# Kernel optimization log

Measured on AMD Instinct MI355X. Metric: run time of the kernel, lower is better.

Reference implementation:

```python
import jax, jax.numpy as jnp
import numpy as np

N, E, IN, H1, H2, C = 50000, 800000, 256, 64, 64, 40
NEG_SLOPE = 0.2


def _glorot(key, shape):
    fan_in = shape[0]
    return jax.random.normal(key, shape, jnp.float32) / np.sqrt(fan_in)


def gat_conv(x, W, al, ar, src, dst, act):
    """DGL-style GATConv (no bias, no residual). al/ar: [H, D]."""
    n = x.shape[0]
    H, D = al.shape
    feat = (x @ W).reshape(n, H, D)                      # [N,H,D]
    el = jnp.sum(feat * al, axis=-1)                     # [N,H]
    er = jnp.sum(feat * ar, axis=-1)                     # [N,H]
    e = jax.nn.leaky_relu(el[src] + er[dst], NEG_SLOPE)  # [E,H]
    # edge softmax over incoming edges of each dst node
    emax = jax.ops.segment_max(e, dst, num_segments=n)
    emax = jnp.where(jnp.isfinite(emax), emax, 0.0)      # guard zero-in-degree
    ex = jnp.exp(e - emax[dst])
    den = jax.ops.segment_sum(ex, dst, num_segments=n)
    alpha = ex / jnp.maximum(den[dst], 1e-9)             # [E,H]
    msg = feat[src] * alpha[..., None]                   # [E,H,D]
    rst = jax.ops.segment_sum(msg, dst, num_segments=n)  # [N,H,D]
    return act(rst) if act is not None else rst


def setup_inputs() -> dict:
    key = jax.random.key(0)
    ks = jax.random.split(key, 24)
    x = jax.random.normal(ks[0], (N, IN), jnp.float32)
    src = jax.random.randint(ks[1], (E,), 0, N, jnp.int32)
    dst = jax.random.randint(ks[2], (E,), 0, N, jnp.int32)
    p = {
        # branch 0 (even): GAT(num_layers=2, heads=[4,1,1])
        "W00": _glorot(ks[3], (IN, 4 * H1)),  "a00l": _glorot(ks[4], (4, H1)),  "a00r": _glorot(ks[5], (4, H1)),
        "W01": _glorot(ks[6], (4 * H1, H1)),  "a01l": _glorot(ks[7], (1, H1)),  "a01r": _glorot(ks[8], (1, H1)),
        "W0f": _glorot(ks[9], (H1, C)),       "a0fl": _glorot(ks[10], (1, C)),  "a0fr": _glorot(ks[11], (1, C)),
        # branch 1 (odd): GAT(num_layers=1, heads=[4,1]) encoder + 1-head output conv
        "W10": _glorot(ks[12], (IN, 4 * H2)), "a10l": _glorot(ks[13], (4, H2)), "a10r": _glorot(ks[14], (4, H2)),
        "W1f": _glorot(ks[15], (4 * H2, H1)), "a1fl": _glorot(ks[16], (1, H1)), "a1fr": _glorot(ks[17], (1, H1)),
        "W1o": _glorot(ks[18], (H1, C)),      "a1ol": _glorot(ks[19], (1, C)),  "a1or": _glorot(ks[20], (1, C)),
    }
    return {"x": x, "src": src, "dst": dst, **p}


def reference(x, src, dst,
              W00, a00l, a00r, W01, a01l, a01r, W0f, a0fl, a0fr,
              W10, a10l, a10r, W1f, a1fl, a1fr, W1o, a1ol, a1or):
    elu = jax.nn.elu
    n = x.shape[0]
    # branch 0: stacked GAT, final layer mean over heads, no activation
    h = gat_conv(x, W00, a00l, a00r, src, dst, elu).reshape(n, -1)   # [N,4*H1]
    h = gat_conv(h, W01, a01l, a01r, src, dst, elu).reshape(n, -1)   # [N,H1]
    y0 = gat_conv(h, W0f, a0fl, a0fr, src, dst, None).mean(axis=1)   # [N,C]
    # branch 1: encoder GAT -> emb, then 1-head output conv with elu
    h = gat_conv(x, W10, a10l, a10r, src, dst, elu).reshape(n, -1)   # [N,4*H2]
    emb = gat_conv(h, W1f, a1fl, a1fr, src, dst, None).mean(axis=1)  # [N,H1]
    y1 = gat_conv(emb, W1o, a1ol, a1or, src, dst, elu)[:, 0, :]      # [N,C]
    return jnp.stack([y0, y1], axis=0)                               # [2,N,C]
```

## Files before the change

### kernel.cpp

```cpp
#include <hip/hip_runtime.h>
#include <math.h>

typedef __attribute__((ext_vector_type(8))) short bf16x8;
typedef __attribute__((ext_vector_type(4))) float f32x4;

#define FMAMIX_LO(acc, pk, s) \
    asm("v_fma_mix_f32 %0, %1, %2, %0 op_sel:[0,0,0] op_sel_hi:[1,0,0]" \
        : "+v"(acc) : "v"(pk), "v"(s))
#define FMAMIX_HI(acc, pk, s) \
    asm("v_fma_mix_f32 %0, %1, %2, %0 op_sel:[1,0,0] op_sel_hi:[1,0,0]" \
        : "+v"(acc) : "v"(pk), "v"(s))

__device__ __forceinline__ unsigned short f2bf(float f) {
    unsigned int u = __float_as_uint(f);
    unsigned int r = (u + 0x7FFF + ((u >> 16) & 1)) >> 16;
    return (unsigned short)r;
}
__device__ __forceinline__ float bf2f(unsigned short h) {
    return __uint_as_float((unsigned int)h << 16);
}
__device__ __forceinline__ void split_bf(float x, unsigned short& hi, unsigned short& lo) {
    hi = f2bf(x);
    lo = f2bf(x - bf2f(hi));
}


__global__ void k_hist(const int* __restrict__ dst, int* __restrict__ deg, int e) {
    int t = blockIdx.x * 256 + threadIdx.x;
    if (t < e) atomicAdd(&deg[dst[t]], 1);
}

__global__ void k_scan1(const int* __restrict__ deg, int* __restrict__ tmp,
                        int* __restrict__ bsum, int n) {
    __shared__ int s[1024];
    int t = threadIdx.x;
    int g = blockIdx.x * 1024 + t;
    int v = (g < n) ? deg[g] : 0;
    s[t] = v;
    __syncthreads();
    for (int off = 1; off < 1024; off <<= 1) {
        int u = (t >= off) ? s[t - off] : 0;
        __syncthreads();
        s[t] += u;
        __syncthreads();
    }
    if (g < n) tmp[g] = s[t];
    if (t == 1023) bsum[blockIdx.x] = s[t];
}

__global__ void k_scan2(int* bsum, int nb) {
    int acc = 0;
    for (int b = 0; b < nb; ++b) { int v = bsum[b]; bsum[b] = acc; acc += v; }
}

__global__ void k_scan3(const int* __restrict__ deg, const int* __restrict__ tmp,
                        const int* __restrict__ bsum, int* __restrict__ rowptr,
                        int* __restrict__ cursor, int n) {
    int g = blockIdx.x * 256 + threadIdx.x;
    if (g < n) {
        int incl = tmp[g] + bsum[g >> 10];
        rowptr[g + 1] = incl;
        cursor[g] = incl - deg[g];
        if (g == 0) rowptr[0] = 0;
    }
}

__global__ void k_scatter(const int* __restrict__ src, const int* __restrict__ dst,
                          int* __restrict__ cursor, int* __restrict__ csr, int e) {
    int t = blockIdx.x * 256 + threadIdx.x;
    if (t < e) {
        int d = dst[t];
        int pos = atomicAdd(&cursor[d], 1);
        csr[pos] = src[t];
    }
}


__global__ void k_castx(const float* __restrict__ x, unsigned short* __restrict__ xhi,
                        unsigned short* __restrict__ xlo, int nvec) {
    int t = blockIdx.x * 256 + threadIdx.x;
    if (t < nvec) {
        float4 v = ((const float4*)x)[t];
        ushort4 h, l;
        split_bf(v.x, h.x, l.x);
        split_bf(v.y, h.y, l.y);
        split_bf(v.z, h.z, l.z);
        split_bf(v.w, h.w, l.w);
        ((ushort4*)xhi)[t] = h;
        ((ushort4*)xlo)[t] = l;
    }
}

__global__ void k_castw(const float* __restrict__ W, unsigned short* __restrict__ Whi,
                        unsigned short* __restrict__ Wlo, int K, int N) {
    int t = blockIdx.x * 256 + threadIdx.x;
    if (t < K * N) {
        int k = t / N, n = t - k * N;
        unsigned short h, l;
        split_bf(W[t], h, l);
        Whi[n * K + k] = h; Wlo[n * K + k] = l;
    }
}


#define LDP 40

__global__ __launch_bounds__(256) void k_gemm_split(const unsigned short* __restrict__ Ahi,
                                                    const unsigned short* __restrict__ Alo,
                                                    const unsigned short* __restrict__ Bhi,
                                                    const unsigned short* __restrict__ Blo,
                                                    _Float16* __restrict__ C,
                                                    int M, int Ncol, int K, int ldc) {
    int bx = blockIdx.x, by = blockIdx.y;
    __shared__ unsigned short Ash[64 * LDP];
    __shared__ unsigned short Asl[64 * LDP];
    __shared__ unsigned short Bsh[64 * LDP];
    __shared__ unsigned short Bsl[64 * LDP];
    int t = threadIdx.x;
    int w = t >> 6, lane = t & 63;
    int lrow = lane & 15, kgrp = (lane >> 4) * 8;
    int row0 = bx * 64, col0 = by * 64;
    int trow = t >> 2, tcol = (t & 3) * 8;

    f32x4 acc[4] = {{0.f, 0.f, 0.f, 0.f}, {0.f, 0.f, 0.f, 0.f},
                    {0.f, 0.f, 0.f, 0.f}, {0.f, 0.f, 0.f, 0.f}};

    for (int k0 = 0; k0 < K; k0 += 32) {
        uint4 ah = {0u,0u,0u,0u}, al = {0u,0u,0u,0u};
        uint4 bh = {0u,0u,0u,0u}, bl = {0u,0u,0u,0u};
        int gr = row0 + trow;
        if (gr < M) {
            ah = *(const uint4*)(Ahi + (size_t)gr * K + k0 + tcol);
            al = *(const uint4*)(Alo + (size_t)gr * K + k0 + tcol);
        }
        int gc = col0 + trow;
        if (gc < Ncol) {
            bh = *(const uint4*)(Bhi + (size_t)gc * K + k0 + tcol);
            bl = *(const uint4*)(Blo + (size_t)gc * K + k0 + tcol);
        }
        __syncthreads();
        *(uint4*)&Ash[trow * LDP + tcol] = ah;
        *(uint4*)&Asl[trow * LDP + tcol] = al;
        *(uint4*)&Bsh[trow * LDP + tcol] = bh;
        *(uint4*)&Bsl[trow * LDP + tcol] = bl;
        __syncthreads();
        bf16x8 vbh = *(const bf16x8*)&Bsh[(w * 16 + lrow) * LDP + kgrp];
        bf16x8 vbl = *(const bf16x8*)&Bsl[(w * 16 + lrow) * LDP + kgrp];
        #pragma unroll
        for (int mt = 0; mt < 4; ++mt) {
            bf16x8 vah = *(const bf16x8*)&Ash[(mt * 16 + lrow) * LDP + kgrp];
            bf16x8 val = *(const bf16x8*)&Asl[(mt * 16 + lrow) * LDP + kgrp];
            acc[mt] = __builtin_amdgcn_mfma_f32_16x16x32_bf16(vah, vbh, acc[mt], 0, 0, 0);
            acc[mt] = __builtin_amdgcn_mfma_f32_16x16x32_bf16(val, vbh, acc[mt], 0, 0, 0);
            acc[mt] = __builtin_amdgcn_mfma_f32_16x16x32_bf16(vah, vbl, acc[mt], 0, 0, 0);
        }
    }

    int ocol = col0 + w * 16 + lrow;
    if (ocol < Ncol) {
        int orow = (lane >> 4) * 4;
        #pragma unroll
        for (int mt = 0; mt < 4; ++mt) {
            #pragma unroll
            for (int r = 0; r < 4; ++r) {
                int m = row0 + mt * 16 + orow + r;
                if (m < M) C[(size_t)m * ldc + ocol] = (_Float16)acc[mt][r];
            }
        }
    }
}

__global__ __launch_bounds__(256) void k_gemm128(const unsigned short* __restrict__ Ahi,
                                                 const unsigned short* __restrict__ Alo,
                                                 const unsigned short* __restrict__ Bhi,
                                                 const unsigned short* __restrict__ Blo,
                                                 _Float16* __restrict__ C,
                                                 int M, int Ncol, int K, int ldc) {
    int Mb = (M + 127) >> 7;
    int nwg = Mb * 2;
    int v = blockIdx.x;
    int q = nwg >> 3, r = nwg & 7;
    int xcd = v & 7, idx = v >> 3;
    int wg = (xcd < r ? xcd * (q + 1) : r * (q + 1) + (xcd - r) * q) + idx;
    int bx = wg >> 1, by = wg & 1;
    int row0 = bx * 128, col0 = by * 128;

    __shared__ unsigned short Ash[128 * LDP];
    __shared__ unsigned short Asl[128 * LDP];
    __shared__ unsigned short Bsh[128 * LDP];
    __shared__ unsigned short Bsl[128 * LDP];

    int t = threadIdx.x;
    int w = t >> 6, lane = t & 63;
    int wr = w >> 1, wc = w & 1;
    int lrow = lane & 15, kgrp = (lane >> 4) * 8;
    int trow = t >> 1, tcol = (t & 1) * 16;

    f32x4 acc[4][4];
    #pragma unroll
    for (int mt = 0; mt < 4; ++mt)
        #pragma unroll
        for (int nt = 0; nt < 4; ++nt)
            acc[mt][nt] = (f32x4){0.f, 0.f, 0.f, 0.f};

    for (int k0 = 0; k0 < K; k0 += 32) {
        uint4 a0 = {0u,0u,0u,0u}, a1 = {0u,0u,0u,0u};
        uint4 l0 = {0u,0u,0u,0u}, l1 = {0u,0u,0u,0u};
        uint4 b0 = {0u,0u,0u,0u}, b1 = {0u,0u,0u,0u};
        uint4 m0 = {0u,0u,0u,0u}, m1 = {0u,0u,0u,0u};
        int gr = row0 + trow;
        if (gr < M) {
            const unsigned short* pa = Ahi + (size_t)gr * K + k0 + tcol;
            const unsigned short* pl = Alo + (size_t)gr * K + k0 + tcol;
            a0 = *(const uint4*)pa;       a1 = *(const uint4*)(pa + 8);
            l0 = *(const uint4*)pl;       l1 = *(const uint4*)(pl + 8);
        }
        int gc = col0 + trow;
        if (gc < Ncol) {
            const unsigned short* pb = Bhi + (size_t)gc * K + k0 + tcol;
            const unsigned short* pm = Blo + (size_t)gc * K + k0 + tcol;
            b0 = *(const uint4*)pb;       b1 = *(const uint4*)(pb + 8);
            m0 = *(const uint4*)pm;       m1 = *(const uint4*)(pm + 8);
        }
        __syncthreads();
        *(uint4*)&Ash[trow * LDP + tcol]     = a0;
        *(uint4*)&Ash[trow * LDP + tcol + 8] = a1;
        *(uint4*)&Asl[trow * LDP + tcol]     = l0;
        *(uint4*)&Asl[trow * LDP + tcol + 8] = l1;
        *(uint4*)&Bsh[trow * LDP + tcol]     = b0;
        *(uint4*)&Bsh[trow * LDP + tcol + 8] = b1;
        *(uint4*)&Bsl[trow * LDP + tcol]     = m0;
        *(uint4*)&Bsl[trow * LDP + tcol + 8] = m1;
        __syncthreads();

        bf16x8 vbh[4], vbl[4];
        #pragma unroll
        for (int nt = 0; nt < 4; ++nt) {
            vbh[nt] = *(const bf16x8*)&Bsh[(wc * 64 + nt * 16 + lrow) * LDP + kgrp];
            vbl[nt] = *(const bf16x8*)&Bsl[(wc * 64 + nt * 16 + lrow) * LDP + kgrp];
        }
        #pragma unroll
        for (int mt = 0; mt < 4; ++mt) {
            bf16x8 vah = *(const bf16x8*)&Ash[(wr * 64 + mt * 16 + lrow) * LDP + kgrp];
            bf16x8 val = *(const bf16x8*)&Asl[(wr * 64 + mt * 16 + lrow) * LDP + kgrp];
            #pragma unroll
            for (int nt = 0; nt < 4; ++nt) {
                acc[mt][nt] = __builtin_amdgcn_mfma_f32_16x16x32_bf16(vah, vbh[nt], acc[mt][nt], 0, 0, 0);
                acc[mt][nt] = __builtin_amdgcn_mfma_f32_16x16x32_bf16(val, vbh[nt], acc[mt][nt], 0, 0, 0);
                acc[mt][nt] = __builtin_amdgcn_mfma_f32_16x16x32_bf16(vah, vbl[nt], acc[mt][nt], 0, 0, 0);
            }
        }
    }

    int orow = (lane >> 4) * 4;
    #pragma unroll
    for (int mt = 0; mt < 4; ++mt) {
        #pragma unroll
        for (int nt = 0; nt < 4; ++nt) {
            int oc = col0 + wc * 64 + nt * 16 + lrow;
            #pragma unroll
            for (int rr = 0; rr < 4; ++rr) {
                int m = row0 + wr * 64 + mt * 16 + orow + rr;
                if (m < M) C[(size_t)m * ldc + oc] = (_Float16)acc[mt][nt][rr];
            }
        }
    }
}

static inline void gemm_split(const unsigned short* Ah, const unsigned short* Al,
                              const unsigned short* Bh, const unsigned short* Bl,
                              _Float16* C, int M, int Ncol, int K, int ldc, hipStream_t st) {
    if (Ncol == 256) {
        int Mb = (M + 127) / 128;
        k_gemm128<<<Mb * 2, 256, 0, st>>>(Ah, Al, Bh, Bl, C, M, Ncol, K, ldc);
    } else {
        int Mb = (M + 63) / 64, Nb = (Ncol + 63) / 64;
        k_gemm_split<<<dim3(Mb, Nb), 256, 0, st>>>(Ah, Al, Bh, Bl, C, M, Ncol, K, ldc);
    }
}


__global__ __launch_bounds__(256) void k_attn4x2(const _Float16* __restrict__ featC,
                                                 const float* __restrict__ a0l,
                                                 const float* __restrict__ a0r,
                                                 const float* __restrict__ a1l,
                                                 const float* __restrict__ a1r,
                                                 float* __restrict__ el8,
                                                 float* __restrict__ er8, int n) {
    int gw = blockIdx.x * 4 + (threadIdx.x >> 6);
    int lane = threadIdx.x & 63;
    int i = gw >> 3;
    if (i >= n) return;
    int rem = gw & 7;
    int b = rem >> 2, h = rem & 3;
    const float* al = b ? a1l : a0l;
    const float* ar = b ? a1r : a0r;
    float f = (float)featC[(size_t)i * 512 + b * 256 + h * 64 + lane];
    float pl = f * al[h * 64 + lane];
    float pr = f * ar[h * 64 + lane];
    #pragma unroll
    for (int off = 32; off; off >>= 1) {
        pl += __shfl_xor(pl, off);
        pr += __shfl_xor(pr, off);
    }
    if (lane == 0) {
        el8[i * 8 + h * 2 + b] = pl;
        er8[i * 8 + h * 2 + b] = pr;
    }
}

template <int DB>
__global__ __launch_bounds__(256) void k_attn2(const _Float16* __restrict__ feat,
                                               const float* __restrict__ al0,
                                               const float* __restrict__ ar0,
                                               const float* __restrict__ al1,
                                               const float* __restrict__ ar1,
                                               float* __restrict__ el2,
                                               float* __restrict__ er2, int n) {
    int gw = blockIdx.x * 4 + (threadIdx.x >> 6);
    int lane = threadIdx.x & 63;
    int i = gw >> 1, b = gw & 1;
    if (i >= n) return;
    bool act = lane < DB;
    float f = act ? (float)feat[(size_t)i * (2 * DB) + b * DB + lane] : 0.f;
    const float* al = b ? al1 : al0;
    const float* ar = b ? ar1 : ar0;
    float pl = act ? f * al[lane] : 0.f;
    float pr = act ? f * ar[lane] : 0.f;
    #pragma unroll
    for (int off = 32; off; off >>= 1) {
        pl += __shfl_xor(pl, off);
        pr += __shfl_xor(pr, off);
    }
    if (lane == 0) {
        el2[i * 2 + b] = pl;
        er2[i * 2 + b] = pr;
    }
}

__device__ __forceinline__ float lrelu(float v) { return v > 0.f ? v : 0.2f * v; }

#define A42_ISSUE(J) uint4 q##J = *(const uint4*)(featLane + ((size_t)(unsigned)__shfl(s, (J) << 2) << 10))
#define A42_CONS(J, X) \
    FMAMIX_LO(f0, q##J.x, X); FMAMIX_HI(f1, q##J.x, X); \
    FMAMIX_LO(f2, q##J.y, X); FMAMIX_HI(f3, q##J.y, X); \
    FMAMIX_LO(f4, q##J.z, X); FMAMIX_HI(f5, q##J.z, X); \
    FMAMIX_LO(f6, q##J.w, X); FMAMIX_HI(f7, q##J.w, X)

__global__ __launch_bounds__(256) void k_agg4x2(const int* __restrict__ rowptr,
                                                const int* __restrict__ csr,
                                                const float* __restrict__ el8,
                                                const float* __restrict__ er8,
                                                const _Float16* __restrict__ featC,
                                                unsigned short* __restrict__ b0hi,
                                                unsigned short* __restrict__ b0lo,
                                                unsigned short* __restrict__ b1hi,
                                                unsigned short* __restrict__ b1lo,
                                                int n) {
    __shared__ float s_ex[4][128];
    int w = threadIdx.x >> 6;
    int lane = threadIdx.x & 63;
    int i = blockIdx.x * 4 + w;
    if (i >= n) return;
    int s0 = rowptr[i], s1 = rowptr[i + 1];
    int deg = s1 - s0;
    int eidx = lane >> 2, h = lane & 3;
    int b = lane >> 5, hh = (lane >> 3) & 3;
    float2 erp = *(const float2*)&er8[i * 8 + h * 2];
    const char* featLane = (const char*)featC + (lane << 4);

    float den0 = 0.f, den1 = 0.f;
    float m0 = -INFINITY, m1 = -INFINITY;
    float f0 = 0.f, f1 = 0.f, f2 = 0.f, f3 = 0.f;
    float f4 = 0.f, f5 = 0.f, f6 = 0.f, f7 = 0.f;

    int e0 = s0 + eidx;
    int s = (e0 < s1) ? csr[e0] : 0;
    for (int c = s0; c < s1; c += 16) {
        bool val = (c + eidx < s1);
        float2 elp = *(const float2*)&el8[(s << 3) + h * 2];
        A42_ISSUE(0);  A42_ISSUE(1);  A42_ISSUE(2);  A42_ISSUE(3);
        A42_ISSUE(4);  A42_ISSUE(5);  A42_ISSUE(6);  A42_ISSUE(7);
        A42_ISSUE(8);  A42_ISSUE(9);  A42_ISSUE(10); A42_ISSUE(11);
        A42_ISSUE(12); A42_ISSUE(13); A42_ISSUE(14); A42_ISSUE(15);
        int en = c + 16 + eidx;
        int sn = (en < s1) ? csr[en] : 0;
        float v0 = val ? lrelu(elp.x + erp.x) : -INFINITY;
        float v1 = val ? lrelu(elp.y + erp.y) : -INFINITY;
        float cm0 = v0, cm1 = v1;
        #pragma unroll
        for (int off = 4; off < 64; off <<= 1) {
            cm0 = fmaxf(cm0, __shfl_xor(cm0, off));
            cm1 = fmaxf(cm1, __shfl_xor(cm1, off));
        }
        float mn0 = fmaxf(m0, cm0), mn1 = fmaxf(m1, cm1);
        float sc0 = __expf(m0 - mn0), sc1 = __expf(m1 - mn1);
        m0 = mn0; m1 = mn1;
        float ex0 = val ? __expf(v0 - mn0) : 0.f;
        float ex1 = val ? __expf(v1 - mn1) : 0.f;
        den0 = den0 * sc0 + ex0;
        den1 = den1 * sc1 + ex1;
        s_ex[w][(h << 4) + eidx] = ex0;
        s_ex[w][64 + (h << 4) + eidx] = ex1;
        float sb0 = __shfl(sc0, hh), sb1 = __shfl(sc1, hh);
        float scl = (lane < 32) ? sb0 : sb1;
        f0 *= scl; f1 *= scl; f2 *= scl; f3 *= scl;
        f4 *= scl; f5 *= scl; f6 *= scl; f7 *= scl;
        const float* exrow = &s_ex[w][(b << 6) + (hh << 4)];
        float4 x0 = *(const float4*)&exrow[0];
        float4 x1 = *(const float4*)&exrow[4];
        float4 x2 = *(const float4*)&exrow[8];
        float4 x3 = *(const float4*)&exrow[12];
        A42_CONS(0, x0.x);  A42_CONS(1, x0.y);  A42_CONS(2, x0.z);  A42_CONS(3, x0.w);
        A42_CONS(4, x1.x);  A42_CONS(5, x1.y);  A42_CONS(6, x1.z);  A42_CONS(7, x1.w);
        A42_CONS(8, x2.x);  A42_CONS(9, x2.y);  A42_CONS(10, x2.z); A42_CONS(11, x2.w);
        A42_CONS(12, x3.x); A42_CONS(13, x3.y); A42_CONS(14, x3.z); A42_CONS(15, x3.w);
        s = sn;
    }

    #pragma unroll
    for (int off = 4; off < 64; off <<= 1) {
        den0 += __shfl_xor(den0, off);
        den1 += __shfl_xor(den1, off);
    }
    float db0 = __shfl(den0, hh), db1 = __shfl(den1, hh);
    float d = fmaxf((lane < 32) ? db0 : db1, 1e-9f);

    float o0 = (deg > 0) ? f0 / d : 0.f;
    float o1 = (deg > 0) ? f1 / d : 0.f;
    float o2 = (deg > 0) ? f2 / d : 0.f;
    float o3 = (deg > 0) ? f3 / d : 0.f;
    float o4 = (deg > 0) ? f4 / d : 0.f;
    float o5 = (deg > 0) ? f5 / d : 0.f;
    float o6 = (deg > 0) ? f6 / d : 0.f;
    float o7 = (deg > 0) ? f7 / d : 0.f;
    o0 = o0 > 0.f ? o0 : (__expf(o0) - 1.f);
    o1 = o1 > 0.f ? o1 : (__expf(o1) - 1.f);
    o2 = o2 > 0.f ? o2 : (__expf(o2) - 1.f);
    o3 = o3 > 0.f ? o3 : (__expf(o3) - 1.f);
    o4 = o4 > 0.f ? o4 : (__expf(o4) - 1.f);
    o5 = o5 > 0.f ? o5 : (__expf(o5) - 1.f);
    o6 = o6 > 0.f ? o6 : (__expf(o6) - 1.f);
    o7 = o7 > 0.f ? o7 : (__expf(o7) - 1.f);

    ushort4 vhA, vlA, vhB, vlB;
    split_bf(o0, vhA.x, vlA.x);
    split_bf(o1, vhA.y, vlA.y);
    split_bf(o2, vhA.z, vlA.z);
    split_bf(o3, vhA.w, vlA.w);
    split_bf(o4, vhB.x, vlB.x);
    split_bf(o5, vhB.y, vlB.y);
    split_bf(o6, vhB.z, vlB.z);
    split_bf(o7, vhB.w, vlB.w);
    size_t base = (size_t)i * 256 + ((lane & 31) << 3);
    if (lane < 32) {
        *(ushort4*)&b0hi[base] = vhA;  *(ushort4*)&b0hi[base + 4] = vhB;
        *(ushort4*)&b0lo[base] = vlA;  *(ushort4*)&b0lo[base + 4] = vlB;
    } else {
        *(ushort4*)&b1hi[base] = vhA;  *(ushort4*)&b1hi[base + 4] = vhB;
        *(ushort4*)&b1lo[base] = vlA;  *(ushort4*)&b1lo[base + 4] = vlB;
    }
}

template <int DB, int ACT0, int ACT1, int SPLITOUT>
__global__ __launch_bounds__(256) void k_agg1x2(const int* __restrict__ rowptr,
                                                const int* __restrict__ csr,
                                                const float* __restrict__ el2,
                                                const float* __restrict__ er2,
                                                const _Float16* __restrict__ featC,
                                                unsigned short* __restrict__ o0hi,
                                                unsigned short* __restrict__ o0lo,
                                                unsigned short* __restrict__ o1hi,
                                                unsigned short* __restrict__ o1lo,
                                                float* __restrict__ ofp0,
                                                float* __restrict__ ofp1, int n) {
    __shared__ int   s_off[4][64];
    __shared__ float s_ex0[4][64];
    __shared__ float s_ex1[4][64];
    int w = threadIdx.x >> 6;
    int i = blockIdx.x * 4 + w;
    int lane = threadIdx.x & 63;
    if (i >= n) return;
    int s0 = rowptr[i], s1 = rowptr[i + 1];
    int deg = s1 - s0;
    float2 erp = *(const float2*)&er2[i * 2];
    bool act = lane < DB;
    int b = (lane >= (DB / 2)) ? 1 : 0;
    int loc = lane - b * (DB / 2);
    const char* featLane = (const char*)featC + lane * 4;
    const int ROWB = 4 * DB;

    float den0 = 0.f, den1 = 0.f, acc0 = 0.f, acc1 = 0.f;
    float m0 = -INFINITY, m1 = -INFINITY;

    auto fma_chunk = [&](int cnt) {
        const float* exr = b ? s_ex1[w] : s_ex0[w];
        int j = 0;
        for (; j + 4 <= cnt; j += 4) {
            int4   oj = *(const int4*)&s_off[w][j];
            float4 xj = *(const float4*)&exr[j];
            unsigned u0 = act ? *(const unsigned*)(featLane + oj.x) : 0u;
            unsigned u1 = act ? *(const unsigned*)(featLane + oj.y) : 0u;
            unsigned u2 = act ? *(const unsigned*)(featLane + oj.z) : 0u;
            unsigned u3 = act ? *(const unsigned*)(featLane + oj.w) : 0u;
            FMAMIX_LO(acc0, u0, xj.x); FMAMIX_HI(acc1, u0, xj.x);
            FMAMIX_LO(acc0, u1, xj.y); FMAMIX_HI(acc1, u1, xj.y);
            FMAMIX_LO(acc0, u2, xj.z); FMAMIX_HI(acc1, u2, xj.z);
            FMAMIX_LO(acc0, u3, xj.w); FMAMIX_HI(acc1, u3, xj.w);
        }
        for (; j < cnt; ++j) {
            unsigned u0 = act ? *(const unsigned*)(featLane + s_off[w][j]) : 0u;
            float x = exr[j];
            FMAMIX_LO(acc0, u0, x); FMAMIX_HI(acc1, u0, x);
        }
    };

    for (int c = s0; c < s1; c += 64) {
        int e = c + lane;
        bool val = e < s1;
        int s = 0;
        float2 elp = {0.f, 0.f};
        if (val) {
            s = csr[e];
            elp = *(const float2*)&el2[s * 2];
        }
        float v0 = val ? lrelu(elp.x + erp.x) : -INFINITY;
        float v1 = val ? lrelu(elp.y + erp.y) : -INFINITY;
        float cm0 = v0, cm1 = v1;
        #pragma unroll
        for (int off = 32; off; off >>= 1) {
            cm0 = fmaxf(cm0, __shfl_xor(cm0, off));
            cm1 = fmaxf(cm1, __shfl_xor(cm1, off));
        }
        float mn0 = fmaxf(m0, cm0), mn1 = fmaxf(m1, cm1);
        float sc0 = __expf(m0 - mn0), sc1 = __expf(m1 - mn1);
        m0 = mn0; m1 = mn1;
        float ex0 = val ? __expf(v0 - mn0) : 0.f;
        float ex1 = val ? __expf(v1 - mn1) : 0.f;
        den0 = den0 * sc0 + ex0;
        den1 = den1 * sc1 + ex1;
        float scl = b ? sc1 : sc0;
        acc0 *= scl; acc1 *= scl;
        s_off[w][lane] = s * ROWB;
        s_ex0[w][lane] = ex0;
        s_ex1[w][lane] = ex1;
        fma_chunk(min(64, s1 - c));
    }
    #pragma unroll
    for (int off = 32; off; off >>= 1) {
        den0 += __shfl_xor(den0, off);
        den1 += __shfl_xor(den1, off);
    }
    float d = fmaxf(b ? den1 : den0, 1e-9f);

    float o0 = (deg > 0) ? acc0 / d : 0.f;
    float o1 = (deg > 0) ? acc1 / d : 0.f;
    int actflag = b ? ACT1 : ACT0;
    if (actflag) {
        o0 = o0 > 0.f ? o0 : (__expf(o0) - 1.f);
        o1 = o1 > 0.f ? o1 : (__expf(o1) - 1.f);
    }
    if (act) {
        if (SPLITOUT) {
            unsigned short h0, l0, h1, l1;
            split_bf(o0, h0, l0);
            split_bf(o1, h1, l1);
            ushort2 vh = {h0, h1}, vl = {l0, l1};
            if (b == 0) {
                *(ushort2*)&o0hi[(size_t)i * DB + 2 * loc] = vh;
                *(ushort2*)&o0lo[(size_t)i * DB + 2 * loc] = vl;
            } else {
                *(ushort2*)&o1hi[(size_t)i * DB + 2 * loc] = vh;
                *(ushort2*)&o1lo[(size_t)i * DB + 2 * loc] = vl;
            }
        } else {
            float2 vo = {o0, o1};
            if (b == 0) *(float2*)&ofp0[(size_t)i * DB + 2 * loc] = vo;
            else        *(float2*)&ofp1[(size_t)i * DB + 2 * loc] = vo;
        }
    }
}


extern "C" void kernel_launch(void* const* d_in, const int* in_sizes, int n_in,
                              void* d_out, int out_size, void* d_ws, size_t ws_size,
                              hipStream_t stream) {
    const float* x    = (const float*)d_in[0];
    const int*   src  = (const int*)d_in[1];
    const int*   dst  = (const int*)d_in[2];
    const float* W00  = (const float*)d_in[3];
    const float* a00l = (const float*)d_in[4];
    const float* a00r = (const float*)d_in[5];
    const float* W01  = (const float*)d_in[6];
    const float* a01l = (const float*)d_in[7];
    const float* a01r = (const float*)d_in[8];
    const float* W0f  = (const float*)d_in[9];
    const float* a0fl = (const float*)d_in[10];
    const float* a0fr = (const float*)d_in[11];
    const float* W10  = (const float*)d_in[12];
    const float* a10l = (const float*)d_in[13];
    const float* a10r = (const float*)d_in[14];
    const float* W1f  = (const float*)d_in[15];
    const float* a1fl = (const float*)d_in[16];
    const float* a1fr = (const float*)d_in[17];
    const float* W1o  = (const float*)d_in[18];
    const float* a1ol = (const float*)d_in[19];
    const float* a1or = (const float*)d_in[20];
    float* out = (float*)d_out;

    const int n = in_sizes[0] / 256;
    const int e = in_sizes[1];
    const int C = 40;

    char* p = (char*)d_ws;
    auto alloc = [&](size_t bytes) -> void* {
        void* r = (void*)p;
        p += (bytes + 255) & ~(size_t)255;
        return r;
    };
    int*   deg     = (int*)alloc((size_t)n * 4);
    int*   tmp     = (int*)alloc((size_t)n * 4);
    int*   bsum    = (int*)alloc(64 * 4);
    int*   rowptr  = (int*)alloc((size_t)(n + 1) * 4);
    int*   cursor  = (int*)alloc((size_t)n * 4);
    int*   csr     = (int*)alloc((size_t)e * 4);
    float* el8     = (float*)alloc((size_t)n * 8 * 4);
    float* er8     = (float*)alloc((size_t)n * 8 * 4);
    _Float16* featC = (_Float16*)alloc((size_t)n * 512 * 2 + 256);
    unsigned short* xhi = (unsigned short*)alloc((size_t)n * 256 * 2);
    unsigned short* xlo = (unsigned short*)alloc((size_t)n * 256 * 2);
    unsigned short* hhi = (unsigned short*)alloc((size_t)n * 256 * 2);
    unsigned short* hlo = (unsigned short*)alloc((size_t)n * 256 * 2);
    unsigned short* W00h = (unsigned short*)alloc(256 * 256 * 2);
    unsigned short* W00l = (unsigned short*)alloc(256 * 256 * 2);
    unsigned short* W01h = (unsigned short*)alloc(256 * 64 * 2);
    unsigned short* W01l = (unsigned short*)alloc(256 * 64 * 2);
    unsigned short* W0fh = (unsigned short*)alloc(64 * 40 * 2);
    unsigned short* W0fl = (unsigned short*)alloc(64 * 40 * 2);
    unsigned short* W10h = (unsigned short*)alloc(256 * 256 * 2);
    unsigned short* W10l = (unsigned short*)alloc(256 * 256 * 2);
    unsigned short* W1fh = (unsigned short*)alloc(256 * 64 * 2);
    unsigned short* W1fl = (unsigned short*)alloc(256 * 64 * 2);
    unsigned short* W1oh = (unsigned short*)alloc(64 * 40 * 2);
    unsigned short* W1ol = (unsigned short*)alloc(64 * 40 * 2);

    hipMemsetAsync(deg, 0, (size_t)n * 4, stream);
    k_hist<<<(e + 255) / 256, 256, 0, stream>>>(dst, deg, e);
    int nb = (n + 1023) / 1024;
    k_scan1<<<nb, 1024, 0, stream>>>(deg, tmp, bsum, n);
    k_scan2<<<1, 1, 0, stream>>>(bsum, nb);
    k_scan3<<<(n + 255) / 256, 256, 0, stream>>>(deg, tmp, bsum, rowptr, cursor, n);
    k_scatter<<<(e + 255) / 256, 256, 0, stream>>>(src, dst, cursor, csr, e);

    int nel = n * 256;
    k_castx<<<(nel / 4 + 255) / 256, 256, 0, stream>>>(x, xhi, xlo, nel / 4);
    k_castw<<<(256 * 256 + 255) / 256, 256, 0, stream>>>(W00, W00h, W00l, 256, 256);
    k_castw<<<(256 * 64 + 255) / 256, 256, 0, stream>>>(W01, W01h, W01l, 256, 64);
    k_castw<<<(64 * 40 + 255) / 256, 256, 0, stream>>>(W0f, W0fh, W0fl, 64, 40);
    k_castw<<<(256 * 256 + 255) / 256, 256, 0, stream>>>(W10, W10h, W10l, 256, 256);
    k_castw<<<(256 * 64 + 255) / 256, 256, 0, stream>>>(W1f, W1fh, W1fl, 256, 64);
    k_castw<<<(64 * 40 + 255) / 256, 256, 0, stream>>>(W1o, W1oh, W1ol, 64, 40);

    int gw1 = (n + 3) / 4;

    gemm_split(xhi, xlo, W00h, W00l, featC,       n, 256, 256, 512, stream);
    gemm_split(xhi, xlo, W10h, W10l, featC + 256, n, 256, 256, 512, stream);
    k_attn4x2<<<(n * 8 + 3) / 4, 256, 0, stream>>>(featC, a00l, a00r, a10l, a10r, el8, er8, n);
    k_agg4x2<<<gw1, 256, 0, stream>>>(rowptr, csr, el8, er8, featC, hhi, hlo, xhi, xlo, n);

    gemm_split(hhi, hlo, W01h, W01l, featC,      n, 64, 256, 128, stream);
    gemm_split(xhi, xlo, W1fh, W1fl, featC + 64, n, 64, 256, 128, stream);
    k_attn2<64><<<(n * 2 + 3) / 4, 256, 0, stream>>>(featC, a01l, a01r, a1fl, a1fr, el8, er8, n);
    k_agg1x2<64, 1, 0, 1><<<gw1, 256, 0, stream>>>(rowptr, csr, el8, er8, featC,
                                                   hhi, hlo, xhi, xlo, nullptr, nullptr, n);

    gemm_split(hhi, hlo, W0fh, W0fl, featC,      n, C, 64, 80, stream);
    gemm_split(xhi, xlo, W1oh, W1ol, featC + 40, n, C, 64, 80, stream);
    k_attn2<40><<<(n * 2 + 3) / 4, 256, 0, stream>>>(featC, a0fl, a0fr, a1ol, a1or, el8, er8, n);
    k_agg1x2<40, 0, 1, 0><<<gw1, 256, 0, stream>>>(rowptr, csr, el8, er8, featC,
                                                   nullptr, nullptr, nullptr, nullptr,
                                                   out, out + (size_t)n * C, n);
}
```

Before: 646.9 us.

## Fuse attention-logit reductions into GEMM epilogues and batch weight casts

Computes el/er (feature dot attention vectors) directly from the fp32 MFMA accumulators in both GEMM kernels, using shuffles plus a small shared-memory cross-wave reduction. This removes the separate k_attn kernels, which had to re-read the fp16 features. It also merges the six weight-cast launches into one segmented kernel. In exchange the logits are now computed from fp32 accumulators rather than fp16-rounded features, and the GEMM epilogue gains extra shuffles and barriers.

Result: faster. 583.6 us (-9.8%).

```diff
diff --git a/kernel.cpp b/kernel.cpp
--- a/kernel.cpp
+++ b/kernel.cpp
@@ -91,15 +91,22 @@
     }
 }
 
-__global__ void k_castw(const float* __restrict__ W, unsigned short* __restrict__ Whi,
-                        unsigned short* __restrict__ Wlo, int K, int N) {
+struct WSeg { const float* W; unsigned short* Wh; unsigned short* Wl; int K; int N; int cnt; };
+__global__ void k_castw_all(WSeg s0, WSeg s1, WSeg s2, WSeg s3, WSeg s4, WSeg s5) {
     int t = blockIdx.x * 256 + threadIdx.x;
-    if (t < K * N) {
-        int k = t / N, n = t - k * N;
-        unsigned short h, l;
-        split_bf(W[t], h, l);
-        Whi[n * K + k] = h; Wlo[n * K + k] = l;
-    }
+    WSeg sg;
+    if      (t < s0.cnt) { sg = s0; }
+    else if ((t -= s0.cnt) < s1.cnt) { sg = s1; }
+    else if ((t -= s1.cnt) < s2.cnt) { sg = s2; }
+    else if ((t -= s2.cnt) < s3.cnt) { sg = s3; }
+    else if ((t -= s3.cnt) < s4.cnt) { sg = s4; }
+    else if ((t -= s4.cnt) < s5.cnt) { sg = s5; }
+    else return;
+    int k = t / sg.N, n = t - k * sg.N;
+    unsigned short h, l;
+    split_bf(sg.W[t], h, l);
+    sg.Wh[n * sg.K + k] = h;
+    sg.Wl[n * sg.K + k] = l;
 }
 
 
@@ -110,7 +117,11 @@
                                                     const unsigned short* __restrict__ Bhi,
                                                     const unsigned short* __restrict__ Blo,
                                                     _Float16* __restrict__ C,
-                                                    int M, int Ncol, int K, int ldc) {
+                                                    int M, int Ncol, int K, int ldc,
+                                                    const float* __restrict__ al,
+                                                    const float* __restrict__ ar,
+                                                    float* __restrict__ el2,
+                                                    float* __restrict__ er2, int bsel) {
     int bx = blockIdx.x, by = blockIdx.y;
     __shared__ unsigned short Ash[64 * LDP];
     __shared__ unsigned short Asl[64 * LDP];
@@ -126,23 +137,23 @@
                     {0.f, 0.f, 0.f, 0.f}, {0.f, 0.f, 0.f, 0.f}};
 
     for (int k0 = 0; k0 < K; k0 += 32) {
-        uint4 ah = {0u,0u,0u,0u}, al = {0u,0u,0u,0u};
-        uint4 bh = {0u,0u,0u,0u}, bl = {0u,0u,0u,0u};
+        uint4 ah = {0u,0u,0u,0u}, al4 = {0u,0u,0u,0u};
+        uint4 bh = {0u,0u,0u,0u}, bl4 = {0u,0u,0u,0u};
         int gr = row0 + trow;
         if (gr < M) {
-            ah = *(const uint4*)(Ahi + (size_t)gr * K + k0 + tcol);
-            al = *(const uint4*)(Alo + (size_t)gr * K + k0 + tcol);
+            ah  = *(const uint4*)(Ahi + (size_t)gr * K + k0 + tcol);
+            al4 = *(const uint4*)(Alo + (size_t)gr * K + k0 + tcol);
         }
         int gc = col0 + trow;
         if (gc < Ncol) {
-            bh = *(const uint4*)(Bhi + (size_t)gc * K + k0 + tcol);
-            bl = *(const uint4*)(Blo + (size_t)gc * K + k0 + tcol);
+            bh  = *(const uint4*)(Bhi + (size_t)gc * K + k0 + tcol);
+            bl4 = *(const uint4*)(Blo + (size_t)gc * K + k0 + tcol);
         }
         __syncthreads();
         *(uint4*)&Ash[trow * LDP + tcol] = ah;
-        *(uint4*)&Asl[trow * LDP + tcol] = al;
+        *(uint4*)&Asl[trow * LDP + tcol] = al4;
         *(uint4*)&Bsh[trow * LDP + tcol] = bh;
-        *(uint4*)&Bsl[trow * LDP + tcol] = bl;
+        *(uint4*)&Bsl[trow * LDP + tcol] = bl4;
         __syncthreads();
         bf16x8 vbh = *(const bf16x8*)&Bsh[(w * 16 + lrow) * LDP + kgrp];
         bf16x8 vbl = *(const bf16x8*)&Bsl[(w * 16 + lrow) * LDP + kgrp];
@@ -157,8 +168,8 @@
     }
 
     int ocol = col0 + w * 16 + lrow;
+    int orow = (lane >> 4) * 4;
     if (ocol < Ncol) {
-        int orow = (lane >> 4) * 4;
         #pragma unroll
         for (int mt = 0; mt < 4; ++mt) {
             #pragma unroll
@@ -168,6 +179,40 @@
             }
         }
     }
+
+    float alv = (ocol < Ncol) ? al[ocol] : 0.f;
+    float arv = (ocol < Ncol) ? ar[ocol] : 0.f;
+    __syncthreads();
+    float* Pl = (float*)Ash;
+    float* Pr = (float*)Bsh;
+    #pragma unroll
+    for (int mt = 0; mt < 4; ++mt) {
+        #pragma unroll
+        for (int r = 0; r < 4; ++r) {
+            float pl = acc[mt][r] * alv;
+            float pr = acc[mt][r] * arv;
+            #pragma unroll
+            for (int off = 1; off < 16; off <<= 1) {
+                pl += __shfl_xor(pl, off);
+                pr += __shfl_xor(pr, off);
+            }
+            if (lrow == 0) {
+                int rloc = mt * 16 + orow + r;
+                Pl[w * 64 + rloc] = pl;
+                Pr[w * 64 + rloc] = pr;
+            }
+        }
+    }
+    __syncthreads();
+    if (t < 64) {
+        int m = row0 + t;
+        if (m < M) {
+            float pl = Pl[t] + Pl[64 + t] + Pl[128 + t] + Pl[192 + t];
+            float pr = Pr[t] + Pr[64 + t] + Pr[128 + t] + Pr[192 + t];
+            el2[m * 2 + bsel] = pl;
+            er2[m * 2 + bsel] = pr;
+        }
+    }
 }
 
 __global__ __launch_bounds__(256) void k_gemm128(const unsigned short* __restrict__ Ahi,
@@ -175,7 +220,11 @@
                                                  const unsigned short* __restrict__ Bhi,
                                                  const unsigned short* __restrict__ Blo,
                                                  _Float16* __restrict__ C,
-                                                 int M, int Ncol, int K, int ldc) {
+                                                 int M, int Ncol, int K, int ldc,
+                                                 const float* __restrict__ al,
+                                                 const float* __restrict__ ar,
+                                                 float* __restrict__ el8,
+                                                 float* __restrict__ er8, int bsel) {
     int Mb = (M + 127) >> 7;
     int nwg = Mb * 2;
     int v = blockIdx.x;
@@ -265,76 +314,52 @@
             }
         }
     }
+
+    int h = by * 2 + wc;
+    float alv[4], arv[4];
+    #pragma unroll
+    for (int nt = 0; nt < 4; ++nt) {
+        int cidx = nt * 16 + lrow;
+        alv[nt] = al[h * 64 + cidx];
+        arv[nt] = ar[h * 64 + cidx];
+    }
+    #pragma unroll
+    for (int mt = 0; mt < 4; ++mt) {
+        #pragma unroll
+        for (int rr = 0; rr < 4; ++rr) {
+            float pl = 0.f, pr = 0.f;
+            #pragma unroll
+            for (int nt = 0; nt < 4; ++nt) {
+                pl = fmaf(acc[mt][nt][rr], alv[nt], pl);
+                pr = fmaf(acc[mt][nt][rr], arv[nt], pr);
+            }
+            #pragma unroll
+            for (int off = 1; off < 16; off <<= 1) {
+                pl += __shfl_xor(pl, off);
+                pr += __shfl_xor(pr, off);
+            }
+            int m = row0 + wr * 64 + mt * 16 + orow + rr;
+            if (lrow == 0 && m < M) {
+                el8[m * 8 + h * 2 + bsel] = pl;
+                er8[m * 8 + h * 2 + bsel] = pr;
+            }
+        }
+    }
 }
 
 static inline void gemm_split(const unsigned short* Ah, const unsigned short* Al,
                               const unsigned short* Bh, const unsigned short* Bl,
-                              _Float16* C, int M, int Ncol, int K, int ldc, hipStream_t st) {
+                              _Float16* C, int M, int Ncol, int K, int ldc,
+                              const float* al, const float* ar,
+                              float* el, float* er, int bsel, hipStream_t st) {
     if (Ncol == 256) {
         int Mb = (M + 127) / 128;
-        k_gemm128<<<Mb * 2, 256, 0, st>>>(Ah, Al, Bh, Bl, C, M, Ncol, K, ldc);
+        k_gemm128<<<Mb * 2, 256, 0, st>>>(Ah, Al, Bh, Bl, C, M, Ncol, K, ldc,
+                                          al, ar, el, er, bsel);
     } else {
         int Mb = (M + 63) / 64, Nb = (Ncol + 63) / 64;
-        k_gemm_split<<<dim3(Mb, Nb), 256, 0, st>>>(Ah, Al, Bh, Bl, C, M, Ncol, K, ldc);
-    }
-}
-
-
-__global__ __launch_bounds__(256) void k_attn4x2(const _Float16* __restrict__ featC,
-                                                 const float* __restrict__ a0l,
-                                                 const float* __restrict__ a0r,
-                                                 const float* __restrict__ a1l,
-                                                 const float* __restrict__ a1r,
-                                                 float* __restrict__ el8,
-                                                 float* __restrict__ er8, int n) {
-    int gw = blockIdx.x * 4 + (threadIdx.x >> 6);
-    int lane = threadIdx.x & 63;
-    int i = gw >> 3;
-    if (i >= n) return;
-    int rem = gw & 7;
-    int b = rem >> 2, h = rem & 3;
-    const float* al = b ? a1l : a0l;
-    const float* ar = b ? a1r : a0r;
-    float f = (float)featC[(size_t)i * 512 + b * 256 + h * 64 + lane];
-    float pl = f * al[h * 64 + lane];
-    float pr = f * ar[h * 64 + lane];
-    #pragma unroll
-    for (int off = 32; off; off >>= 1) {
-        pl += __shfl_xor(pl, off);
-        pr += __shfl_xor(pr, off);
-    }
-    if (lane == 0) {
-        el8[i * 8 + h * 2 + b] = pl;
-        er8[i * 8 + h * 2 + b] = pr;
-    }
-}
-
-template <int DB>
-__global__ __launch_bounds__(256) void k_attn2(const _Float16* __restrict__ feat,
-                                               const float* __restrict__ al0,
-                                               const float* __restrict__ ar0,
-                                               const float* __restrict__ al1,
-                                               const float* __restrict__ ar1,
-                                               float* __restrict__ el2,
-                                               float* __restrict__ er2, int n) {
-    int gw = blockIdx.x * 4 + (threadIdx.x >> 6);
-    int lane = threadIdx.x & 63;
-    int i = gw >> 1, b = gw & 1;
-    if (i >= n) return;
-    bool act = lane < DB;
-    float f = act ? (float)feat[(size_t)i * (2 * DB) + b * DB + lane] : 0.f;
-    const float* al = b ? al1 : al0;
-    const float* ar = b ? ar1 : ar0;
-    float pl = act ? f * al[lane] : 0.f;
-    float pr = act ? f * ar[lane] : 0.f;
-    #pragma unroll
-    for (int off = 32; off; off >>= 1) {
-        pl += __shfl_xor(pl, off);
-        pr += __shfl_xor(pr, off);
-    }
-    if (lane == 0) {
-        el2[i * 2 + b] = pl;
-        er2[i * 2 + b] = pr;
+        k_gemm_split<<<dim3(Mb, Nb), 256, 0, st>>>(Ah, Al, Bh, Bl, C, M, Ncol, K, ldc,
+                                                   al, ar, el, er, bsel);
     }
 }
 
@@ -654,29 +679,36 @@
 
     int nel = n * 256;
     k_castx<<<(nel / 4 + 255) / 256, 256, 0, stream>>>(x, xhi, xlo, nel / 4);
-    k_castw<<<(256 * 256 + 255) / 256, 256, 0, stream>>>(W00, W00h, W00l, 256, 256);
-    k_castw<<<(256 * 64 + 255) / 256, 256, 0, stream>>>(W01, W01h, W01l, 256, 64);
-    k_castw<<<(64 * 40 + 255) / 256, 256, 0, stream>>>(W0f, W0fh, W0fl, 64, 40);
-    k_castw<<<(256 * 256 + 255) / 256, 256, 0, stream>>>(W10, W10h, W10l, 256, 256);
-    k_castw<<<(256 * 64 + 255) / 256, 256, 0, stream>>>(W1f, W1fh, W1fl, 256, 64);
-    k_castw<<<(64 * 40 + 255) / 256, 256, 0, stream>>>(W1o, W1oh, W1ol, 64, 40);
+    {
+        WSeg s0 = {W00, W00h, W00l, 256, 256, 256 * 256};
+        WSeg s1 = {W10, W10h, W10l, 256, 256, 256 * 256};
+        WSeg s2 = {W01, W01h, W01l, 256, 64, 256 * 64};
+        WSeg s3 = {W1f, W1fh, W1fl, 256, 64, 256 * 64};
+        WSeg s4 = {W0f, W0fh, W0fl, 64, 40, 64 * 40};
+        WSeg s5 = {W1o, W1oh, W1ol, 64, 40, 64 * 40};
+        int tot = 2 * 65536 + 2 * 16384 + 2 * 2560;
+        k_castw_all<<<(tot + 255) / 256, 256, 0, stream>>>(s0, s1, s2, s3, s4, s5);
+    }
 
     int gw1 = (n + 3) / 4;
 
-    gemm_split(xhi, xlo, W00h, W00l, featC,       n, 256, 256, 512, stream);
-    gemm_split(xhi, xlo, W10h, W10l, featC + 256, n, 256, 256, 512, stream);
-    k_attn4x2<<<(n * 8 + 3) / 4, 256, 0, stream>>>(featC, a00l, a00r, a10l, a10r, el8, er8, n);
+    gemm_split(xhi, xlo, W00h, W00l, featC,       n, 256, 256, 512,
+               a00l, a00r, el8, er8, 0, stream);
+    gemm_split(xhi, xlo, W10h, W10l, featC + 256, n, 256, 256, 512,
+               a10l, a10r, el8, er8, 1, stream);
     k_agg4x2<<<gw1, 256, 0, stream>>>(rowptr, csr, el8, er8, featC, hhi, hlo, xhi, xlo, n);
 
-    gemm_split(hhi, hlo, W01h, W01l, featC,      n, 64, 256, 128, stream);
-    gemm_split(xhi, xlo, W1fh, W1fl, featC + 64, n, 64, 256, 128, stream);
-    k_attn2<64><<<(n * 2 + 3) / 4, 256, 0, stream>>>(featC, a01l, a01r, a1fl, a1fr, el8, er8, n);
+    gemm_split(hhi, hlo, W01h, W01l, featC,      n, 64, 256, 128,
+               a01l, a01r, el8, er8, 0, stream);
+    gemm_split(xhi, xlo, W1fh, W1fl, featC + 64, n, 64, 256, 128,
+               a1fl, a1fr, el8, er8, 1, stream);
     k_agg1x2<64, 1, 0, 1><<<gw1, 256, 0, stream>>>(rowptr, csr, el8, er8, featC,
                                                    hhi, hlo, xhi, xlo, nullptr, nullptr, n);
 
-    gemm_split(hhi, hlo, W0fh, W0fl, featC,      n, C, 64, 80, stream);
-    gemm_split(xhi, xlo, W1oh, W1ol, featC + 40, n, C, 64, 80, stream);
-    k_attn2<40><<<(n * 2 + 3) / 4, 256, 0, stream>>>(featC, a0fl, a0fr, a1ol, a1or, el8, er8, n);
+    gemm_split(hhi, hlo, W0fh, W0fl, featC,      n, C, 64, 80,
+               a0fl, a0fr, el8, er8, 0, stream);
+    gemm_split(xhi, xlo, W1oh, W1ol, featC + 40, n, C, 64, 80,
+               a1ol, a1or, el8, er8, 1, stream);
     k_agg1x2<40, 0, 1, 0><<<gw1, 256, 0, stream>>>(rowptr, csr, el8, er8, featC,
                                                    nullptr, nullptr, nullptr, nullptr,
                                                    out, out + (size_t)n * C, n);
```
